# Optimization experiments

Hardware: AMD Instinct MI355X
Metric: run time of the kernel (lower is better)

Reference implementation:

```python
import jax, jax.numpy as jnp
import numpy as np

T, N = 256, 128
STATE_D, TARGET_D = 64, 64
HID = 512
A, P = 8, 8
AP = A * P
REPEAT = 2
THR = 1.0  # snntorch default threshold


@jax.custom_vjp
def spike(x):
    # Heaviside with ATan surrogate gradient (snntorch default, alpha=2)
    return (x > 0.0).astype(x.dtype)

def _spike_fwd(x):
    return (x > 0.0).astype(x.dtype), x

def _spike_bwd(x, g):
    return (g / (1.0 + (jnp.pi * x) ** 2),)

spike.defvjp(_spike_fwd, _spike_bwd)


def setup_inputs() -> dict:
    key = jax.random.key(0)
    ks = jax.random.split(key, 16)
    in_dim = STATE_D + TARGET_D
    g = lambda k, shape, fan: (jax.random.uniform(k, shape, jnp.float32) * 2.0 - 1.0) / np.sqrt(fan)
    return {
        "state": jax.random.normal(ks[0], (T, N, STATE_D), jnp.float32),
        "target": jax.random.normal(ks[1], (T, N, TARGET_D), jnp.float32),
        "W_rec_in": g(ks[2], (HID, in_dim), in_dim),
        "b_rec_in": jnp.zeros((HID,), jnp.float32),
        "W_rec": g(ks[3], (HID, HID), HID),
        "b_rec": jnp.zeros((HID,), jnp.float32),
        "alpha_rec": jax.random.uniform(ks[4], (HID,), jnp.float32),
        "beta_rec": jax.random.uniform(ks[5], (HID,), jnp.float32),
        "W_ff_in": g(ks[6], (HID, HID), HID),
        "b_ff_in": jnp.zeros((HID,), jnp.float32),
        "alpha_ff": jax.random.uniform(ks[7], (HID,), jnp.float32),
        "beta_ff": jax.random.uniform(ks[8], (HID,), jnp.float32),
        "W_mu_in": g(ks[9], (AP, HID), HID),
        "b_mu_in": jnp.zeros((AP,), jnp.float32),
        "beta_mu": jax.random.uniform(ks[10], (AP,), jnp.float32),
        "W_mu_out": jnp.full((A, AP), 1.0 / P, jnp.float32),
        "W_lv_in": g(ks[11], (AP, HID), HID),
        "b_lv_in": jnp.zeros((AP,), jnp.float32),
        "beta_lv": jax.random.uniform(ks[12], (AP,), jnp.float32),
        "W_lv_out": jnp.full((A, AP), 1.0 / P, jnp.float32),
    }


def _forward(state, target, W_rec_in, b_rec_in, W_rec, b_rec, alpha_rec, beta_rec,
             W_ff_in, b_ff_in, alpha_ff, beta_ff,
             W_mu_in, b_mu_in, beta_mu, W_mu_out,
             W_lv_in, b_lv_in, beta_lv, W_lv_out):
    x_all = jnp.concatenate([state, target], axis=-1)  # [T, N, in_dim]

    def neuron_step(carry, x):
        spk_r, syn_r, mem_r, syn_f, mem_f, mem_mu, mem_lv = carry
        # --- RSynaptic (recurrent LIF with synaptic current), reset=subtract ---
        cur_r = x @ W_rec_in.T + b_rec_in + spk_r @ W_rec.T + b_rec
        reset_r = jax.lax.stop_gradient((mem_r > THR).astype(x.dtype))
        syn_r = alpha_rec * syn_r + cur_r
        mem_r = beta_rec * mem_r + syn_r - reset_r * THR
        spk_r = spike(mem_r - THR)
        # --- Synaptic feed-forward layer, reset=subtract ---
        cur_f = spk_r @ W_ff_in.T + b_ff_in
        reset_f = jax.lax.stop_gradient((mem_f > THR).astype(x.dtype))
        syn_f = alpha_ff * syn_f + cur_f
        mem_f = beta_ff * mem_f + syn_f - reset_f * THR
        spk_f = spike(mem_f - THR)
        # --- readout Synaptic neurons: alpha=0 (syn == input), reset='none' ---
        mem_mu = beta_mu * mem_mu + (spk_f @ W_mu_in.T + b_mu_in)
        mem_lv = beta_lv * mem_lv + (spk_f @ W_lv_in.T + b_lv_in)
        mu = mem_mu @ W_mu_out.T   # [N, A]
        lv = mem_lv @ W_lv_out.T   # [N, A]
        return (spk_r, syn_r, mem_r, syn_f, mem_f, mem_mu, mem_lv), (mu, lv)

    def t_step(carry, x):
        mus, lvs = [], []
        for _ in range(REPEAT):  # repeat_input, fixed and small
            carry, (mu, lv) = neuron_step(carry, x)
            mus.append(mu)
            lvs.append(lv)
        return carry, (jnp.mean(jnp.stack(mus), 0), jnp.mean(jnp.stack(lvs), 0))

    z = jnp.zeros((N, HID), state.dtype)
    z2 = jnp.zeros((N, AP), state.dtype)
    carry0 = (z, z, z, z, z, z2, z2)
    _, (mu_outs, lv_outs) = jax.lax.scan(t_step, carry0, x_all)
    return mu_outs, lv_outs  # each [T, N, A]


def reference(state, target, W_rec_in, b_rec_in, W_rec, b_rec, alpha_rec, beta_rec,
              W_ff_in, b_ff_in, alpha_ff, beta_ff,
              W_mu_in, b_mu_in, beta_mu, W_mu_out,
              W_lv_in, b_lv_in, beta_lv, W_lv_out):
    return _forward(state, target, W_rec_in, b_rec_in, W_rec, b_rec, alpha_rec, beta_rec,
                    W_ff_in, b_ff_in, alpha_ff, beta_ff,
                    W_mu_in, b_mu_in, beta_mu, W_mu_out,
                    W_lv_in, b_lv_in, beta_lv, W_lv_out)
```

## Files before the change

### kernel.cpp

```cpp
#include <hip/hip_runtime.h>


typedef unsigned int       u32;
typedef unsigned short     u16;
typedef unsigned long long u64;
typedef unsigned char      u8;

#define TSTEPS 512
#define HIDDEN 512

#define XW_OFF    0ull
#define C3_OFF    0ull
#define MEM_OFF   33554432ull
#define SPKB_OFF  100663296ull
#define WT_OFF    109051904ull
#define WINT_OFF  109314048ull
#define RING_OFF  134217728ull
#define CNT_OFF   134742016ull
#define WS_NEED   (134742016ull + 4096ull)

#define QCHUNK 384

__global__ __launch_bounds__(256) void k_prepT(
    const float* __restrict__ Win,
    const float* __restrict__ Wmu, const float* __restrict__ Wlv,
    float* __restrict__ WinT, float* __restrict__ WT)
{
  const int idx = blockIdx.x * 256 + threadIdx.x;
  if (idx < 65536) {
    const int k = idx >> 9, j = idx & 511;
    WinT[idx] = Win[j * 128 + k];
  } else {
    const int i2 = idx - 65536;
    const int k = i2 >> 7, j = i2 & 127;
    WT[i2] = (j < 64) ? Wmu[j * 512 + k] : Wlv[(j - 64) * 512 + k];
  }
}

__global__ __launch_bounds__(256) void k_xw(
    const float* __restrict__ state, const float* __restrict__ target,
    const float* __restrict__ WinT, const float* __restrict__ b_in,
    float* __restrict__ XW)
{
  __shared__ float xs[16][129];
  const int tid  = threadIdx.x;
  const int row0 = blockIdx.x * 16;

  for (int e = tid; e < 2048; e += 256) {
    int r = e >> 7, k = e & 127;
    xs[r][k] = (k < 64) ? state[(row0 + r) * 64 + k]
                        : target[(row0 + r) * 64 + k - 64];
  }
  __syncthreads();

#pragma unroll
  for (int jh = 0; jh < 2; ++jh) {
    const int j = jh * 256 + tid;
    float acc[16];
#pragma unroll
    for (int r = 0; r < 16; ++r) acc[r] = 0.0f;
    for (int k = 0; k < 128; ++k) {
      const float wv = WinT[k * 512 + j];
#pragma unroll
      for (int r = 0; r < 16; ++r)
        acc[r] = __builtin_fmaf(xs[r][k], wv, acc[r]);
    }
    const float b = b_in[j];
#pragma unroll
    for (int r = 0; r < 16; ++r)
      XW[(row0 + r) * 512 + j] = __fadd_rn(acc[r], b);
  }
}

__global__ __launch_bounds__(256, 1) void k_rec(
    const float* __restrict__ XW,
    const float* __restrict__ Wrec, const float* __restrict__ Wff,
    const float* __restrict__ alpha_rec, const float* __restrict__ beta_rec,
    const float* __restrict__ b_rec,
    const float* __restrict__ b_ff, const float* __restrict__ alpha_ff,
    const float* __restrict__ beta_ff,
    u32* __restrict__ ring32, u32* __restrict__ spkb32)
{
  __shared__ float WR[16 * 516];
  __shared__ float WF[16 * 516];
  __shared__ u32   Bits[2][16][17];

  const int tid  = threadIdx.x;
  const int g    = blockIdx.x & 7;
  const int c    = blockIdx.x >> 3;
  const int n0   = g * 16;
  const int wv   = tid >> 6;
  const int lane = tid & 63;
  const int ch   = lane & 15;
  const int rp   = lane >> 4;
  const int rowb = 8 * (wv & 1) + 2 * rp;
  const bool isFF = (wv >= 2);
  const int jj   = c * 16 + ch;

  for (int it = tid; it < 2048; it += 256) {
    const int r16 = it >> 7, k4 = (it & 127) * 4;
    *(float4*)(WR + r16 * 516 + k4) = *(const float4*)(Wrec + (c * 16 + r16) * 512 + k4);
    *(float4*)(WF + r16 * 516 + k4) = *(const float4*)(Wff  + (c * 16 + r16) * 512 + k4);
  }

  float coA, coB, coC;
  if (!isFF) { coA = alpha_rec[jj]; coB = beta_rec[jj]; coC = b_rec[jj]; }
  else       { coA = alpha_ff[jj];  coB = beta_ff[jj];  coC = b_ff[jj]; }

  float syn[2] = {0.f, 0.f}, mem[2] = {0.f, 0.f}, spk[2] = {0.f, 0.f};

  const float* wp = (isFF ? WF : WR) + ch * 516;
  const int srow = tid >> 4;
  const int sjl  = tid & 15;

  __syncthreads();

  for (int tp = 0; tp <= TSTEPS; ++tp) {
    float xw[2] = {0.f, 0.f};
    if (!isFF && tp < TSTEPS) {
      const float* ph = XW + ((tp >> 1) * 128 + n0 + rowb) * 512 + jj;
      xw[0] = ph[0];
      xw[1] = ph[512];
    }

    float SA[2] = {0.f, 0.f};

    if (tp > 0) {
      const int bp = (tp - 1) & 1;
      {
        const u32 exp = (u32)(tp - 1);
        const u32* src = ring32 + (bp * 128 + n0 + srow) * 32 + 2 * sjl;
        u32 m0 = __hip_atomic_load(src,     __ATOMIC_RELAXED, __HIP_MEMORY_SCOPE_AGENT);
        while ((m0 >> 16) != exp) {
          __builtin_amdgcn_s_sleep(1);
          m0 = __hip_atomic_load(src,     __ATOMIC_RELAXED, __HIP_MEMORY_SCOPE_AGENT);
        }
        u32 m1 = __hip_atomic_load(src + 1, __ATOMIC_RELAXED, __HIP_MEMORY_SCOPE_AGENT);
        while ((m1 >> 16) != exp) {
          __builtin_amdgcn_s_sleep(1);
          m1 = __hip_atomic_load(src + 1, __ATOMIC_RELAXED, __HIP_MEMORY_SCOPE_AGENT);
        }
        Bits[bp][srow][sjl] = (m0 & 0xFFFFu) | (m1 << 16);
      }
      __syncthreads();

      if (isFF || tp < TSTEPS) {
        float a0A = 0.f, a0B = 0.f, a1A = 0.f, a1B = 0.f;
        for (int kb = 0; kb < 12; ++kb) {
          const u32 w0 = Bits[bp][rowb][kb];
          const u32 w1 = Bits[bp][rowb + 1][kb];
#pragma unroll
          for (int k4 = 0; k4 < 32; k4 += 4) {
            const float4 w4 = *(const float4*)(wp + kb * 32 + k4);
#pragma unroll
            for (int i = 0; i < 4; ++i) {
              const float wvv = (i == 0) ? w4.x : (i == 1) ? w4.y : (i == 2) ? w4.z : w4.w;
              a0A = __builtin_fmaf((float)((w0 >> (k4 + i)) & 1u), wvv, a0A);
              a1A = __builtin_fmaf((float)((w1 >> (k4 + i)) & 1u), wvv, a1A);
            }
          }
        }
        for (int kb = 12; kb < 16; ++kb) {
          const u32 w0 = Bits[bp][rowb][kb];
          const u32 w1 = Bits[bp][rowb + 1][kb];
#pragma unroll
          for (int k4 = 0; k4 < 32; k4 += 4) {
            const float4 w4 = *(const float4*)(wp + kb * 32 + k4);
#pragma unroll
            for (int i = 0; i < 4; ++i) {
              const float wvv = (i == 0) ? w4.x : (i == 1) ? w4.y : (i == 2) ? w4.z : w4.w;
              a0B = __builtin_fmaf((float)((w0 >> (k4 + i)) & 1u), wvv, a0B);
              a1B = __builtin_fmaf((float)((w1 >> (k4 + i)) & 1u), wvv, a1B);
            }
          }
        }
        SA[0] = __fadd_rn(a0A, a0B);
        SA[1] = __fadd_rn(a1A, a1B);
      }
    }

    if (isFF) {
      if (tp > 0) {
#pragma unroll
        for (int i = 0; i < 2; ++i) {
          float curf = __fadd_rn(SA[i], coC);
          syn[i] = __fadd_rn(__fmul_rn(coA, syn[i]), curf);
          mem[i] = __fsub_rn(__fadd_rn(__fmul_rn(coB, mem[i]), syn[i]), spk[i]);
          spk[i] = (mem[i] > 1.0f) ? 1.0f : 0.0f;
        }
        const u64 B0 = __ballot(spk[0] != 0.f);
        const u64 B1 = __ballot(spk[1] != 0.f);
        if (ch == 0) {
          const u64 base = ((u64)(tp - 1) * 128 + n0 + rowb) * 32 + c;
          __hip_atomic_store(spkb32 + base,      (u32)((B0 >> (16 * rp)) & 0xFFFFull),
                             __ATOMIC_RELAXED, __HIP_MEMORY_SCOPE_AGENT);
          __hip_atomic_store(spkb32 + base + 32, (u32)((B1 >> (16 * rp)) & 0xFFFFull),
                             __ATOMIC_RELAXED, __HIP_MEMORY_SCOPE_AGENT);
        }
      }
    } else {
      if (tp < TSTEPS) {
#pragma unroll
        for (int i = 0; i < 2; ++i) {
          float cur = __fadd_rn(__fadd_rn(xw[i], SA[i]), coC);
          syn[i] = __fadd_rn(__fmul_rn(coA, syn[i]), cur);
          mem[i] = __fsub_rn(__fadd_rn(__fmul_rn(coB, mem[i]), syn[i]), spk[i]);
          spk[i] = (mem[i] > 1.0f) ? 1.0f : 0.0f;
        }
        const u64 B0 = __ballot(spk[0] != 0.f);
        const u64 B1 = __ballot(spk[1] != 0.f);
        if (ch == 0) {
          const u32 tag = ((u32)tp) << 16;
          const int base = ((tp & 1) * 128 + n0 + rowb) * 32 + c;
          __hip_atomic_store(ring32 + base,
                             tag | (u32)((B0 >> (16 * rp)) & 0xFFFFull),
                             __ATOMIC_RELAXED, __HIP_MEMORY_SCOPE_AGENT);
          __hip_atomic_store(ring32 + base + 32,
                             tag | (u32)((B1 >> (16 * rp)) & 0xFFFFull),
                             __ATOMIC_RELAXED, __HIP_MEMORY_SCOPE_AGENT);
        }
      }
    }
  }
}

__global__ __launch_bounds__(256) void k_c3(
    const u32* __restrict__ spkb32, const float* __restrict__ WT,
    const float* __restrict__ bmu, const float* __restrict__ blv,
    float* __restrict__ c3)
{
  __shared__ u32 Bc[32][32];
  const int tid  = threadIdx.x;
  const int rows0 = blockIdx.x * 32;

  for (int it = tid; it < 1024; it += 256)
    ((u32*)Bc)[it] = spkb32[(u64)rows0 * 32 + it];
  __syncthreads();

  const int j  = tid & 127;
  const int rh = tid >> 7;
  const float bias = (j < 64) ? bmu[j] : blv[j - 64];

  float accA[16], accB[16];
#pragma unroll
  for (int r = 0; r < 16; ++r) { accA[r] = 0.f; accB[r] = 0.f; }

  for (int m = 0; m < 24; ++m) {
    u32 wrow[16];
#pragma unroll
    for (int r = 0; r < 16; ++r) wrow[r] = Bc[rh * 16 + r][m];
    const float* wpp = WT + (m * 16) * 128 + j;
#pragma unroll
    for (int kk = 0; kk < 16; ++kk) {
      const float wvv = wpp[kk * 128];
#pragma unroll
      for (int r = 0; r < 16; ++r) {
        const float b = (float)((wrow[r] >> kk) & 1u);
        accA[r] = __builtin_fmaf(b, wvv, accA[r]);
      }
    }
  }
  for (int m = 24; m < 32; ++m) {
    u32 wrow[16];
#pragma unroll
    for (int r = 0; r < 16; ++r) wrow[r] = Bc[rh * 16 + r][m];
    const float* wpp = WT + (m * 16) * 128 + j;
#pragma unroll
    for (int kk = 0; kk < 16; ++kk) {
      const float wvv = wpp[kk * 128];
#pragma unroll
      for (int r = 0; r < 16; ++r) {
        const float b = (float)((wrow[r] >> kk) & 1u);
        accB[r] = __builtin_fmaf(b, wvv, accB[r]);
      }
    }
  }

#pragma unroll
  for (int r = 0; r < 16; ++r)
    c3[(u64)(rows0 + rh * 16 + r) * 128 + j] =
        __fadd_rn(__fadd_rn(accA[r], accB[r]), bias);
}

__global__ __launch_bounds__(256) void k_scan(
    const float* __restrict__ c3,
    const float* __restrict__ beta_mu, const float* __restrict__ beta_lv,
    float* __restrict__ Mem)
{
  const int tid = blockIdx.x * 256 + threadIdx.x;
  const int n = tid >> 7, ap = tid & 127;
  const float beta = (ap < 64) ? beta_mu[ap] : beta_lv[ap - 64];
  const float* src = c3 + n * 128 + ap;
  float* dst = Mem + n * 128 + ap;
  float mem = 0.0f;
  for (int t = 0; t < 512; ++t) {
    mem = __fadd_rn(__fmul_rn(beta, mem), src[(u64)t * 16384]);
    dst[(u64)t * 16384] = mem;
  }
}

__global__ __launch_bounds__(256) void k_out(
    const float* __restrict__ Mem,
    const float* __restrict__ Wmu_out, const float* __restrict__ Wlv_out,
    float* __restrict__ out)
{
  const int tid = blockIdx.x * 256 + threadIdx.x;
  const int a = tid & 7;
  const int n = (tid >> 3) & 127;
  const int t = (tid >> 10) & 255;
  const int kind = tid >> 18;
  const float* wv = ((kind == 0) ? Wmu_out : Wlv_out) + a * 64;
  const float* s0 = Mem + ((u64)(2 * t) * 128 + n) * 128 + kind * 64;
  const float* s1 = Mem + ((u64)(2 * t + 1) * 128 + n) * 128 + kind * 64;
  float mu0 = 0.0f, mu1 = 0.0f;
#pragma unroll 8
  for (int q = 0; q < 64; ++q) mu0 = __builtin_fmaf(s0[q], wv[q], mu0);
#pragma unroll 8
  for (int q = 0; q < 64; ++q) mu1 = __builtin_fmaf(s1[q], wv[q], mu1);
  out[tid] = __fmul_rn(__fadd_rn(mu0, mu1), 0.5f);
}

extern "C" void kernel_launch(void* const* d_in, const int* in_sizes, int n_in,
                              void* d_out, int out_size, void* d_ws, size_t ws_size,
                              hipStream_t stream) {
  (void)in_sizes; (void)n_in; (void)out_size;
  if (ws_size < WS_NEED) return;

  const float* state     = (const float*)d_in[0];
  const float* target    = (const float*)d_in[1];
  const float* W_rec_in  = (const float*)d_in[2];
  const float* b_rec_in  = (const float*)d_in[3];
  const float* W_rec     = (const float*)d_in[4];
  const float* b_rec     = (const float*)d_in[5];
  const float* alpha_rec = (const float*)d_in[6];
  const float* beta_rec  = (const float*)d_in[7];
  const float* W_ff_in   = (const float*)d_in[8];
  const float* b_ff_in   = (const float*)d_in[9];
  const float* alpha_ff  = (const float*)d_in[10];
  const float* beta_ff   = (const float*)d_in[11];
  const float* W_mu_in   = (const float*)d_in[12];
  const float* b_mu_in   = (const float*)d_in[13];
  const float* beta_mu   = (const float*)d_in[14];
  const float* W_mu_out  = (const float*)d_in[15];
  const float* W_lv_in   = (const float*)d_in[16];
  const float* b_lv_in   = (const float*)d_in[17];
  const float* beta_lv   = (const float*)d_in[18];
  const float* W_lv_out  = (const float*)d_in[19];

  char* ws = (char*)d_ws;
  float* XW    = (float*)(ws + XW_OFF);
  float* c3    = (float*)(ws + C3_OFF);
  float* Mem   = (float*)(ws + MEM_OFF);
  u32*   spkb32= (u32*)  (ws + SPKB_OFF);
  float* WT    = (float*)(ws + WT_OFF);
  float* WinT  = (float*)(ws + WINT_OFF);
  u32*   ring32= (u32*)  (ws + RING_OFF);

  hipLaunchKernelGGL(k_prepT, dim3(512), dim3(256), 0, stream,
                     W_rec_in, W_mu_in, W_lv_in, WinT, WT);
  hipLaunchKernelGGL(k_xw, dim3(2048), dim3(256), 0, stream,
                     state, target, WinT, b_rec_in, XW);
  hipLaunchKernelGGL(k_rec, dim3(256), dim3(256), 0, stream,
                     XW, W_rec, W_ff_in,
                     alpha_rec, beta_rec, b_rec,
                     b_ff_in, alpha_ff, beta_ff, ring32, spkb32);
  hipLaunchKernelGGL(k_c3, dim3(2048), dim3(256), 0, stream,
                     spkb32, WT, b_mu_in, b_lv_in, c3);
  hipLaunchKernelGGL(k_scan, dim3(64), dim3(256), 0, stream,
                     c3, beta_mu, beta_lv, Mem);
  hipLaunchKernelGGL(k_out, dim3(2048), dim3(256), 0, stream,
                     Mem, W_mu_out, W_lv_out, (float*)d_out);
}
```

Baseline: 4.888 ms.

## Double k_rec block size so each thread computes one row per step

The recurrent kernel moves from 256 to 512 threads per block, so each lane handles one batch row instead of two. This halves the serial FMA chain per thread in the spike-weighted matvec, and XW is now loaded only on even steps. The ring protocol is reworked to one 16-bit word per thread, with the tag set to tp+1 so a zero-initialised ring is never read as valid. It also switches the spkb32 writes to plain stores and raises the launch bounds to two blocks per CU. The cost is more waves taking part in each per-step barrier and spin-wait, plus tighter register limits.

```diff
diff --git a/kernel.cpp b/kernel.cpp
--- a/kernel.cpp
+++ b/kernel.cpp
@@ -72,7 +72,7 @@
   }
 }
 
-__global__ __launch_bounds__(256, 1) void k_rec(
+__global__ __launch_bounds__(512, 2) void k_rec(
     const float* __restrict__ XW,
     const float* __restrict__ Wrec, const float* __restrict__ Wff,
     const float* __restrict__ alpha_rec, const float* __restrict__ beta_rec,
@@ -83,7 +83,7 @@
 {
   __shared__ float WR[16 * 516];
   __shared__ float WF[16 * 516];
-  __shared__ u32   Bits[2][16][17];
+  __shared__ u32   BitsW[2][16][17];
 
   const int tid  = threadIdx.x;
   const int g    = blockIdx.x & 7;
@@ -92,12 +92,12 @@
   const int wv   = tid >> 6;
   const int lane = tid & 63;
   const int ch   = lane & 15;
-  const int rp   = lane >> 4;
-  const int rowb = 8 * (wv & 1) + 2 * rp;
-  const bool isFF = (wv >= 2);
+  const int rloc = lane >> 4;
+  const int row  = (wv & 3) * 4 + rloc;
+  const bool isFF = (wv >= 4);
   const int jj   = c * 16 + ch;
 
-  for (int it = tid; it < 2048; it += 256) {
+  for (int it = tid; it < 2048; it += 512) {
     const int r16 = it >> 7, k4 = (it & 127) * 4;
     *(float4*)(WR + r16 * 516 + k4) = *(const float4*)(Wrec + (c * 16 + r16) * 512 + k4);
     *(float4*)(WF + r16 * 516 + k4) = *(const float4*)(Wff  + (c * 16 + r16) * 512 + k4);
@@ -107,116 +107,87 @@
   if (!isFF) { coA = alpha_rec[jj]; coB = beta_rec[jj]; coC = b_rec[jj]; }
   else       { coA = alpha_ff[jj];  coB = beta_ff[jj];  coC = b_ff[jj]; }
 
-  float syn[2] = {0.f, 0.f}, mem[2] = {0.f, 0.f}, spk[2] = {0.f, 0.f};
+  float syn = 0.f, mem = 0.f, spk = 0.f, xw = 0.f;
 
   const float* wp = (isFF ? WF : WR) + ch * 516;
-  const int srow = tid >> 4;
-  const int sjl  = tid & 15;
+  const int srow = tid >> 5;
+  const int sjl  = tid & 31;
 
   __syncthreads();
 
   for (int tp = 0; tp <= TSTEPS; ++tp) {
-    float xw[2] = {0.f, 0.f};
-    if (!isFF && tp < TSTEPS) {
-      const float* ph = XW + ((tp >> 1) * 128 + n0 + rowb) * 512 + jj;
-      xw[0] = ph[0];
-      xw[1] = ph[512];
-    }
-
-    float SA[2] = {0.f, 0.f};
+    if (!isFF && tp < TSTEPS && !(tp & 1))
+      xw = XW[((tp >> 1) * 128 + n0 + row) * 512 + jj];
+
+    float SA = 0.f;
 
     if (tp > 0) {
       const int bp = (tp - 1) & 1;
       {
-        const u32 exp = (u32)(tp - 1);
-        const u32* src = ring32 + (bp * 128 + n0 + srow) * 32 + 2 * sjl;
-        u32 m0 = __hip_atomic_load(src,     __ATOMIC_RELAXED, __HIP_MEMORY_SCOPE_AGENT);
-        while ((m0 >> 16) != exp) {
+        const u32 expct = (u32)tp;
+        const u32* src = ring32 + (bp * 128 + n0 + srow) * 32 + sjl;
+        u32 m = __hip_atomic_load(src, __ATOMIC_RELAXED, __HIP_MEMORY_SCOPE_AGENT);
+        while ((m >> 16) != expct) {
           __builtin_amdgcn_s_sleep(1);
-          m0 = __hip_atomic_load(src,     __ATOMIC_RELAXED, __HIP_MEMORY_SCOPE_AGENT);
-        }
-        u32 m1 = __hip_atomic_load(src + 1, __ATOMIC_RELAXED, __HIP_MEMORY_SCOPE_AGENT);
-        while ((m1 >> 16) != exp) {
-          __builtin_amdgcn_s_sleep(1);
-          m1 = __hip_atomic_load(src + 1, __ATOMIC_RELAXED, __HIP_MEMORY_SCOPE_AGENT);
-        }
-        Bits[bp][srow][sjl] = (m0 & 0xFFFFu) | (m1 << 16);
+          m = __hip_atomic_load(src, __ATOMIC_RELAXED, __HIP_MEMORY_SCOPE_AGENT);
+        }
+        ((u16*)BitsW[bp][srow])[sjl] = (u16)m;
       }
       __syncthreads();
 
       if (isFF || tp < TSTEPS) {
-        float a0A = 0.f, a0B = 0.f, a1A = 0.f, a1B = 0.f;
+        float aA = 0.f, aB = 0.f;
         for (int kb = 0; kb < 12; ++kb) {
-          const u32 w0 = Bits[bp][rowb][kb];
-          const u32 w1 = Bits[bp][rowb + 1][kb];
+          const u32 w0 = BitsW[bp][row][kb];
 #pragma unroll
           for (int k4 = 0; k4 < 32; k4 += 4) {
             const float4 w4 = *(const float4*)(wp + kb * 32 + k4);
 #pragma unroll
             for (int i = 0; i < 4; ++i) {
               const float wvv = (i == 0) ? w4.x : (i == 1) ? w4.y : (i == 2) ? w4.z : w4.w;
-              a0A = __builtin_fmaf((float)((w0 >> (k4 + i)) & 1u), wvv, a0A);
-              a1A = __builtin_fmaf((float)((w1 >> (k4 + i)) & 1u), wvv, a1A);
+              aA = __builtin_fmaf((float)((w0 >> (k4 + i)) & 1u), wvv, aA);
             }
           }
         }
         for (int kb = 12; kb < 16; ++kb) {
-          const u32 w0 = Bits[bp][rowb][kb];
-          const u32 w1 = Bits[bp][rowb + 1][kb];
+          const u32 w0 = BitsW[bp][row][kb];
 #pragma unroll
           for (int k4 = 0; k4 < 32; k4 += 4) {
             const float4 w4 = *(const float4*)(wp + kb * 32 + k4);
 #pragma unroll
             for (int i = 0; i < 4; ++i) {
               const float wvv = (i == 0) ? w4.x : (i == 1) ? w4.y : (i == 2) ? w4.z : w4.w;
-              a0B = __builtin_fmaf((float)((w0 >> (k4 + i)) & 1u), wvv, a0B);
-              a1B = __builtin_fmaf((float)((w1 >> (k4 + i)) & 1u), wvv, a1B);
+              aB = __builtin_fmaf((float)((w0 >> (k4 + i)) & 1u), wvv, aB);
             }
           }
         }
-        SA[0] = __fadd_rn(a0A, a0B);
-        SA[1] = __fadd_rn(a1A, a1B);
+        SA = __fadd_rn(aA, aB);
       }
     }
 
     if (isFF) {
       if (tp > 0) {
-#pragma unroll
-        for (int i = 0; i < 2; ++i) {
-          float curf = __fadd_rn(SA[i], coC);
-          syn[i] = __fadd_rn(__fmul_rn(coA, syn[i]), curf);
-          mem[i] = __fsub_rn(__fadd_rn(__fmul_rn(coB, mem[i]), syn[i]), spk[i]);
-          spk[i] = (mem[i] > 1.0f) ? 1.0f : 0.0f;
-        }
-        const u64 B0 = __ballot(spk[0] != 0.f);
-        const u64 B1 = __ballot(spk[1] != 0.f);
+        float curf = __fadd_rn(SA, coC);
+        syn = __fadd_rn(__fmul_rn(coA, syn), curf);
+        mem = __fsub_rn(__fadd_rn(__fmul_rn(coB, mem), syn), spk);
+        spk = (mem > 1.0f) ? 1.0f : 0.0f;
+        const u64 B = __ballot(spk != 0.f);
         if (ch == 0) {
-          const u64 base = ((u64)(tp - 1) * 128 + n0 + rowb) * 32 + c;
-          __hip_atomic_store(spkb32 + base,      (u32)((B0 >> (16 * rp)) & 0xFFFFull),
-                             __ATOMIC_RELAXED, __HIP_MEMORY_SCOPE_AGENT);
-          __hip_atomic_store(spkb32 + base + 32, (u32)((B1 >> (16 * rp)) & 0xFFFFull),
-                             __ATOMIC_RELAXED, __HIP_MEMORY_SCOPE_AGENT);
+          spkb32[((u64)(tp - 1) * 128 + n0 + row) * 32 + c] =
+              (u32)((B >> (16 * rloc)) & 0xFFFFull);
         }
       }
     } else {
       if (tp < TSTEPS) {
-#pragma unroll
-        for (int i = 0; i < 2; ++i) {
-          float cur = __fadd_rn(__fadd_rn(xw[i], SA[i]), coC);
-          syn[i] = __fadd_rn(__fmul_rn(coA, syn[i]), cur);
-          mem[i] = __fsub_rn(__fadd_rn(__fmul_rn(coB, mem[i]), syn[i]), spk[i]);
-          spk[i] = (mem[i] > 1.0f) ? 1.0f : 0.0f;
-        }
-        const u64 B0 = __ballot(spk[0] != 0.f);
-        const u64 B1 = __ballot(spk[1] != 0.f);
+        float cur = __fadd_rn(__fadd_rn(xw, SA), coC);
+        syn = __fadd_rn(__fmul_rn(coA, syn), cur);
+        mem = __fsub_rn(__fadd_rn(__fmul_rn(coB, mem), syn), spk);
+        spk = (mem > 1.0f) ? 1.0f : 0.0f;
+        const u64 B = __ballot(spk != 0.f);
         if (ch == 0) {
-          const u32 tag = ((u32)tp) << 16;
-          const int base = ((tp & 1) * 128 + n0 + rowb) * 32 + c;
-          __hip_atomic_store(ring32 + base,
-                             tag | (u32)((B0 >> (16 * rp)) & 0xFFFFull),
-                             __ATOMIC_RELAXED, __HIP_MEMORY_SCOPE_AGENT);
-          __hip_atomic_store(ring32 + base + 32,
-                             tag | (u32)((B1 >> (16 * rp)) & 0xFFFFull),
+          const u32 tag = ((u32)(tp + 1)) << 16;
+          __hip_atomic_store(ring32 + ((tp & 1) * 128 + n0 + row) * 32 + c,
+                             tag | (u32)((B >> (16 * rloc)) & 0xFFFFull),
                              __ATOMIC_RELAXED, __HIP_MEMORY_SCOPE_AGENT);
         }
       }
@@ -360,7 +331,7 @@
                      W_rec_in, W_mu_in, W_lv_in, WinT, WT);
   hipLaunchKernelGGL(k_xw, dim3(2048), dim3(256), 0, stream,
                      state, target, WinT, b_rec_in, XW);
-  hipLaunchKernelGGL(k_rec, dim3(256), dim3(256), 0, stream,
+  hipLaunchKernelGGL(k_rec, dim3(256), dim3(512), 0, stream,
                      XW, W_rec, W_ff_in,
                      alpha_rec, beta_rec, b_rec,
                      b_ff_in, alpha_ff, beta_ff, ring32, spkb32);
```

New measurement: 4.152 ms. 15.1% less time.
